# Performance work log

Measured on AMD Instinct MI355X. Metric: run time of the kernel, lower is better.

## Reference

```python
import jax, jax.numpy as jnp
import numpy as np

EMBED, HIDDEN, VOCAB = 512, 512, 30000
B, S, K, NT = 16, 128, 49, 5


def _lin(x, W, b):
    # torch nn.Linear: y = x @ W.T + b, W stored as (out, in)
    return x @ W.T + b


def setup_inputs() -> dict:
    key = jax.random.key(0)
    ks = jax.random.split(key, 32)
    g = lambda i, shape, scale=0.05: (jax.random.normal(ks[i], shape, dtype=jnp.float32) * scale)
    inp = {
        "epoch": 30,
        "h_t": jax.random.normal(ks[0], (B, S, HIDDEN), dtype=jnp.float32),
        "V": jax.random.normal(ks[1], (B, K, HIDDEN), dtype=jnp.float32),
        "T": jax.random.normal(ks[2], (B, NT, EMBED), dtype=jnp.float32),
        "W_ZV": g(3, (49, HIDDEN)), "b_ZV": jnp.zeros((49,), jnp.float32),
        "W_Zh": g(4, (49, HIDDEN)), "b_Zh": jnp.zeros((49,), jnp.float32),
        "W_az": g(5, (1, 49)), "b_az": jnp.zeros((1,), jnp.float32),
        "W_QT": g(6, (5, EMBED)), "b_QT": jnp.zeros((5,), jnp.float32),
        "W_Qh": g(7, (5, HIDDEN)), "b_Qh": jnp.zeros((5,), jnp.float32),
        "W_bq": g(8, (1, 5)), "b_bq": jnp.zeros((1,), jnp.float32),
        "W_sq": g(9, (EMBED, EMBED)), "b_sq": jnp.zeros((EMBED,), jnp.float32),
        "W_sh": g(10, (EMBED, HIDDEN)), "b_sh": jnp.zeros((EMBED,), jnp.float32),
        "W_Ss": g(11, (5, EMBED)), "b_Ss": jnp.zeros((5,), jnp.float32),
        "W_Sr": g(12, (5, EMBED)), "b_Sr": jnp.zeros((5,), jnp.float32),
        "W_sz": g(13, (EMBED, HIDDEN)), "b_sz": jnp.zeros((EMBED,), jnp.float32),
        "W_mlp": g(14, (VOCAB, EMBED)), "b_mlp": jnp.zeros((VOCAB,), jnp.float32),
    }
    return inp


def reference(epoch, h_t, V, T,
              W_ZV, b_ZV, W_Zh, b_Zh, W_az, b_az,
              W_QT, b_QT, W_Qh, b_Qh, W_bq, b_bq,
              W_sq, b_sq, W_sh, b_sh, W_Ss, b_Ss,
              W_Sr, b_Sr, W_sz, b_sz, W_mlp, b_mlp):
    # --- visual attention (dropout = identity, eval mode) ---
    # content_V: [B, S, K, 49]
    content_V = _lin(V, W_ZV, b_ZV)[:, None, :, :] + _lin(h_t, W_Zh, b_Zh)[:, :, None, :]
    visual_t = (jnp.tanh(content_V) @ W_az.T + b_az)[..., 0]          # [B, S, K]
    alpha_t = jax.nn.softmax(visual_t, axis=-1)
    z_t = jnp.einsum('bsk,bkh->bsh', alpha_t, V)                      # [B, S, H]
    r_t = jnp.tanh(_lin(z_t, W_sz, b_sz))                             # [B, S, E]
    # --- topic attention ---
    content_T = _lin(T, W_QT, b_QT)[:, None, :, :] + _lin(h_t, W_Qh, b_Qh)[:, :, None, :]  # [B,S,5,5]
    topic_t = (jnp.tanh(content_T) @ W_bq.T + b_bq)[..., 0]           # [B, S, 5]
    beta_t = jax.nn.softmax(topic_t, axis=-1)
    q_t = jnp.einsum('bst,bte->bse', beta_t, T)                       # [B, S, E]
    s_t = jnp.tanh(_lin(q_t, W_sq, b_sq) + _lin(h_t, W_sh, b_sh))     # [B, S, E]
    # --- sentinel scores: the torch loop reduces to (batch 0, diagonal pos) only ---
    qh0 = _lin(h_t[0], W_Qh, b_Qh)                                    # [S, 5]
    score_s = jnp.tanh(_lin(s_t[0], W_Ss, b_Ss) + qh0) @ W_bq.T + b_bq  # [S, 1]
    score_r = jnp.tanh(_lin(r_t[0], W_Sr, b_Sr) + qh0) @ W_bq.T + b_bq  # [S, 1]
    if epoch <= 20:
        gama_t = 1.0
    else:
        gama_t = jax.nn.sigmoid(score_s - score_r)[None, :, :]        # [1, S, 1]
    c_t = gama_t * s_t + (1.0 - gama_t) * r_t                         # [B, S, E]
    scores = _lin(c_t, W_mlp, b_mlp)                                  # [B, S, vocab]
    return scores
```

## Files before the change

### kernel.cpp

```cpp
#include <hip/hip_runtime.h>
#include <hip/hip_bf16.h>


typedef short bf16x8 __attribute__((ext_vector_type(8)));
typedef float f32x4 __attribute__((ext_vector_type(4)));
typedef short short8 __attribute__((ext_vector_type(8)));

static __device__ __forceinline__ short f2bf(float f) {
    union { float f; unsigned u; } v; v.f = f;
    unsigned r = v.u + 0x7FFFu + ((v.u >> 16) & 1u);
    return (short)(r >> 16);
}

#define GLD_LDS16(gp, lp)                                                          \
    __builtin_amdgcn_global_load_lds(                                              \
        (const __attribute__((address_space(1))) unsigned int*)(gp),               \
        (__attribute__((address_space(3))) unsigned int*)(lp), 16, 0, 0)

__global__ __launch_bounds__(256) void k_front(
    const float* __restrict__ h, const float* __restrict__ V, const float* __restrict__ T,
    const float* __restrict__ W_Zh, const float* __restrict__ W_Qh,
    const float* __restrict__ W_ZV, const float* __restrict__ W_QT,
    short* __restrict__ P1, short* __restrict__ P2, short* __restrict__ P3,
    short* __restrict__ V_b, short* __restrict__ T_b, short* __restrict__ h_b,
    const float* __restrict__ wsz, short* __restrict__ wsz_b,
    const float* __restrict__ wsq, short* __restrict__ wsq_b,
    const float* __restrict__ wsh, short* __restrict__ wsh_b,
    const float* __restrict__ wmlp, short* __restrict__ wmlp_b)
{
    const int bid = blockIdx.x;
    const int t = threadIdx.x;

    if (bid < 48) {
        const int pid = bid >> 4, blk = bid & 15;
        short* dst = (pid == 0) ? P1 : (pid == 1) ? P2 : P3;
        const int base = blk * 2048 + t * 8;
        const int r = base >> 9, c = base & 511;
        const float* srow = nullptr;
        if (pid == 0)      srow = (r < 49) ? (W_Zh + r * 512) : ((r < 54) ? (W_Qh + (r - 49) * 512) : nullptr);
        else if (pid == 1) srow = (r < 49) ? (W_ZV + r * 512) : nullptr;
        else               srow = (r < 5)  ? (W_QT + r * 512) : nullptr;
        short8 o = {0, 0, 0, 0, 0, 0, 0, 0};
        if (srow) {
            const float4 a = *(const float4*)(srow + c);
            const float4 b = *(const float4*)(srow + c + 4);
            o[0] = f2bf(a.x); o[1] = f2bf(a.y); o[2] = f2bf(a.z); o[3] = f2bf(a.w);
            o[4] = f2bf(b.x); o[5] = f2bf(b.y); o[6] = f2bf(b.z); o[7] = f2bf(b.w);
        }
        *(short8*)(dst + base) = o;
        return;
    }
    const float* src; short* dst; int i;
    if (bid < 244)       { src = V;    dst = V_b;    i = (bid - 48) * 256 + t; }
    else if (bid < 264)  { src = T;    dst = T_b;    i = (bid - 244) * 256 + t; }
    else if (bid < 776)  { src = h;    dst = h_b;    i = (bid - 264) * 256 + t; }
    else if (bid < 904)  { src = wsz;  dst = wsz_b;  i = (bid - 776) * 256 + t; }
    else if (bid < 1032) { src = wsq;  dst = wsq_b;  i = (bid - 904) * 256 + t; }
    else if (bid < 1160) { src = wsh;  dst = wsh_b;  i = (bid - 1032) * 256 + t; }
    else                 { src = wmlp; dst = wmlp_b; i = (bid - 1160) * 256 + t; }
    const float4 a = ((const float4*)src)[i * 2];
    const float4 b = ((const float4*)src)[i * 2 + 1];
    short8 o;
    o[0] = f2bf(a.x); o[1] = f2bf(a.y); o[2] = f2bf(a.z); o[3] = f2bf(a.w);
    o[4] = f2bf(b.x); o[5] = f2bf(b.y); o[6] = f2bf(b.z); o[7] = f2bf(b.w);
    ((short8*)dst)[i] = o;
}

__global__ __launch_bounds__(256) void k_linhv(
    const short* __restrict__ h_b, const short* __restrict__ V_b, const short* __restrict__ T_b,
    const short* __restrict__ P1, const short* __restrict__ P2, const short* __restrict__ P3,
    const float* __restrict__ b_Zh, const float* __restrict__ b_Qh,
    const float* __restrict__ b_ZV, const float* __restrict__ b_QT,
    float* __restrict__ Zh, float* __restrict__ Qh,
    float* __restrict__ ZV, float* __restrict__ QT)
{
    constexpr int K = 512;
    const int bid = blockIdx.x;
    int sect, m0;
    const short *Ag, *Wg;
    if (bid < 32)      { sect = 0; m0 = bid * 64;        Ag = h_b; Wg = P1; }
    else if (bid < 45) { sect = 1; m0 = (bid - 32) * 64; Ag = V_b; Wg = P2; }
    else               { sect = 2; m0 = (bid - 45) * 64; Ag = T_b; Wg = P3; }

    __shared__ __align__(16) short sA[64 * 64];
    __shared__ __align__(16) short sW[64 * 64];
    const int tid = threadIdx.x;
    const int l = tid & 63, w = tid >> 6;
    const int wm = (w & 1) * 32, wn = (w >> 1) * 32;
    const int lm = l & 15, lg = l >> 4;
    const int sr = l >> 3, sc = l & 7;
    f32x4 acc[2][2] = {};

    for (int k0 = 0; k0 < K; k0 += 64) {
        #pragma unroll
        for (int c = 0; c < 2; ++c) {
            const int R = w * 16 + c * 8;
            const int row = R + sr;
            GLD_LDS16(Ag + (size_t)(m0 + row) * K + k0 + ((sc ^ (row & 7)) << 3), sA + R * 64);
            GLD_LDS16(Wg + (size_t)row * K + k0 + ((sc ^ (row & 7)) << 3), sW + R * 64);
        }
        __syncthreads();
        bf16x8 af[2][2], bv[2][2];
        #pragma unroll
        for (int s = 0; s < 2; ++s)
            #pragma unroll
            for (int i = 0; i < 2; ++i) {
                const int ra = wm + i * 16 + lm;
                const int rb = wn + i * 16 + lm;
                af[s][i] = *(const bf16x8*)(sA + ra * 64 + (((s * 4 + lg) ^ (ra & 7)) << 3));
                bv[s][i] = *(const bf16x8*)(sW + rb * 64 + (((s * 4 + lg) ^ (rb & 7)) << 3));
            }
        #pragma unroll
        for (int s = 0; s < 2; ++s)
            #pragma unroll
            for (int i = 0; i < 2; ++i)
                #pragma unroll
                for (int j = 0; j < 2; ++j)
                    acc[i][j] = __builtin_amdgcn_mfma_f32_16x16x32_bf16(af[s][i], bv[s][j], acc[i][j], 0, 0, 0);
        __syncthreads();
    }

    #pragma unroll
    for (int j = 0; j < 2; ++j) {
        const int n = wn + j * 16 + lm;
        #pragma unroll
        for (int i = 0; i < 2; ++i) {
            #pragma unroll
            for (int q = 0; q < 4; ++q) {
                const int m = m0 + wm + i * 16 + lg * 4 + q;
                const float v = acc[i][j][q];
                if (sect == 0) {
                    if (n < 49)      Zh[(size_t)m * 64 + n] = v + b_Zh[n];
                    else if (n < 54) Qh[(size_t)m * 8 + (n - 49)] = v + b_Qh[n - 49];
                } else if (sect == 1) {
                    if (m < 784 && n < 49) ZV[(size_t)m * 64 + n] = v + b_ZV[n];
                } else {
                    if (m < 80 && n < 5) QT[(size_t)m * 8 + n] = v + b_QT[n];
                }
            }
        }
    }
}

__global__ void k_attn(const float* __restrict__ V, const float* __restrict__ T,
                       const float* __restrict__ ZV, const float* __restrict__ Zh,
                       const float* __restrict__ QT, const float* __restrict__ Qh,
                       const float* __restrict__ W_az, const float* __restrict__ b_az,
                       const float* __restrict__ W_bq, const float* __restrict__ b_bq,
                       short* __restrict__ z_bf, short* __restrict__ q_bf)
{
    const int row = blockIdx.x;
    const int b = row >> 7;
    const int t = threadIdx.x;
    __shared__ float zh[49], waz[49], alpha[49], beta[5];
    if (t < 49) { zh[t] = Zh[row * 64 + t]; waz[t] = W_az[t]; }
    __syncthreads();
    if (t < 49) {
        const float* zv = ZV + (b * 49 + t) * 64;
        float acc = b_az[0];
        for (int j = 0; j < 49; ++j) acc += tanhf(zv[j] + zh[j]) * waz[j];
        alpha[t] = acc;
    } else if (t >= 64 && t < 69) {
        const int tt = t - 64;
        const float* qt = QT + (b * 5 + tt) * 8;
        const float* qh = Qh + row * 8;
        float acc = b_bq[0];
        for (int j = 0; j < 5; ++j) acc += tanhf(qt[j] + qh[j]) * W_bq[j];
        beta[tt] = acc;
    }
    __syncthreads();
    const int wv = t >> 6, l = t & 63;
    if (wv == 0) {
        float a = (l < 49) ? alpha[l] : -1e30f;
        float m = a;
        #pragma unroll
        for (int off = 32; off; off >>= 1) m = fmaxf(m, __shfl_xor(m, off));
        float e = (l < 49) ? expf(a - m) : 0.f;
        float s = e;
        #pragma unroll
        for (int off = 32; off; off >>= 1) s += __shfl_xor(s, off);
        if (l < 49) alpha[l] = e / s;
    } else if (wv == 1) {
        float a = (l < 5) ? beta[l] : -1e30f;
        float m = a;
        #pragma unroll
        for (int off = 32; off; off >>= 1) m = fmaxf(m, __shfl_xor(m, off));
        float e = (l < 5) ? expf(a - m) : 0.f;
        float s = e;
        #pragma unroll
        for (int off = 32; off; off >>= 1) s += __shfl_xor(s, off);
        if (l < 5) beta[l] = e / s;
    }
    __syncthreads();
    const float* Vb = V + (size_t)b * 49 * 512;
    const float* Tb = T + (size_t)b * 5 * 512;
    for (int hd = t; hd < 512; hd += 256) {
        float az = 0.f;
        #pragma unroll
        for (int k = 0; k < 49; ++k) az = fmaf(alpha[k], Vb[k * 512 + hd], az);
        z_bf[(size_t)row * 512 + hd] = f2bf(az);
        float aq = 0.f;
        #pragma unroll
        for (int k = 0; k < 5; ++k) aq = fmaf(beta[k], Tb[k * 512 + hd], aq);
        q_bf[(size_t)row * 512 + hd] = f2bf(aq);
    }
}

__global__ __launch_bounds__(256) void k_rs(
    const short* __restrict__ Zb, const short* __restrict__ Qb, const short* __restrict__ Hb,
    const short* __restrict__ Wsz, const short* __restrict__ Wsq, const short* __restrict__ Wsh,
    const float* __restrict__ b_sz, const float* __restrict__ b_sq, const float* __restrict__ b_sh,
    float* __restrict__ r_t, float* __restrict__ s_t)
{
    constexpr int K = 512, NN = 512;
    __shared__ __align__(16) short sA[64 * 64];
    __shared__ __align__(16) short sW[64 * 64];
    const int tid = threadIdx.x;
    const int l = tid & 63, w = tid >> 6;
    const int m0 = blockIdx.x * 64, n0 = blockIdx.y * 64;
    const int wm = (w & 1) * 32, wn = (w >> 1) * 32;
    const int lm = l & 15, lg = l >> 4;
    const int sr = l >> 3, sc = l & 7;
    f32x4 accr[2][2] = {}, accs[2][2] = {};

#define RS_PASS(AG, WG, ACC)                                                      \
    for (int k0 = 0; k0 < K; k0 += 64) {                                          \
        _Pragma("unroll")                                                         \
        for (int c = 0; c < 2; ++c) {                                             \
            const int R = w * 16 + c * 8;                                         \
            const int row = R + sr;                                               \
            GLD_LDS16((AG) + (size_t)(m0 + row) * K + k0 + ((sc ^ (row & 7)) << 3), sA + R * 64); \
            GLD_LDS16((WG) + (size_t)(n0 + row) * K + k0 + ((sc ^ (row & 7)) << 3), sW + R * 64); \
        }                                                                         \
        __syncthreads();                                                          \
        bf16x8 af[2][2], bv[2][2];                                                \
        _Pragma("unroll")                                                         \
        for (int s = 0; s < 2; ++s)                                               \
            _Pragma("unroll")                                                     \
            for (int i = 0; i < 2; ++i) {                                         \
                const int ra = wm + i * 16 + lm;                                  \
                const int rb = wn + i * 16 + lm;                                  \
                af[s][i] = *(const bf16x8*)(sA + ra * 64 + (((s * 4 + lg) ^ (ra & 7)) << 3)); \
                bv[s][i] = *(const bf16x8*)(sW + rb * 64 + (((s * 4 + lg) ^ (rb & 7)) << 3)); \
            }                                                                     \
        _Pragma("unroll")                                                         \
        for (int s = 0; s < 2; ++s)                                               \
            _Pragma("unroll")                                                     \
            for (int i = 0; i < 2; ++i)                                           \
                _Pragma("unroll")                                                 \
                for (int j = 0; j < 2; ++j)                                       \
                    ACC[i][j] = __builtin_amdgcn_mfma_f32_16x16x32_bf16(af[s][i], bv[s][j], ACC[i][j], 0, 0, 0); \
        __syncthreads();                                                          \
    }

    RS_PASS(Zb, Wsz, accr)
    RS_PASS(Qb, Wsq, accs)
    RS_PASS(Hb, Wsh, accs)
#undef RS_PASS

    #pragma unroll
    for (int j = 0; j < 2; ++j) {
        const int n = n0 + wn + j * 16 + lm;
        const float br = b_sz[n];
        const float bs = b_sq[n] + b_sh[n];
        #pragma unroll
        for (int i = 0; i < 2; ++i) {
            const int m = m0 + wm + i * 16 + lg * 4;
            #pragma unroll
            for (int q = 0; q < 4; ++q) {
                r_t[(size_t)(m + q) * NN + n] = tanhf(accr[i][j][q] + br);
                s_t[(size_t)(m + q) * NN + n] = tanhf(accs[i][j][q] + bs);
            }
        }
    }
}

__global__ __launch_bounds__(256, 4) void k_gemm_mlp(
    const short* __restrict__ A, const short* __restrict__ Wb,
    const float* __restrict__ bias, float* __restrict__ C)
{
    constexpr int N = 30000, K = 512;
    __shared__ __align__(16) short shA[128 * 64];
    __shared__ __align__(16) short shW[128 * 64];
    const int tid = threadIdx.x;
    const int l = tid & 63, w = tid >> 6;
    const int bid = blockIdx.x;
    const int swz = (bid & 7) * 470 + (bid >> 3);
    const int m0 = (swz & 15) * 128;
    const int n0 = (swz >> 4) * 128;
    const int wm = (w & 1) * 64, wn = (w >> 1) * 64;
    const int lm = l & 15, lg = l >> 4;
    const int sr = tid >> 3, sc = tid & 7;
    const short* Ag = A  + (size_t)m0 * K;
    const short* Wg = Wb + (size_t)n0 * K;
    f32x4 acc[4][4] = {};

    for (int t = 0; t < 8; ++t) {
        const int kk = t * 64;
        #pragma unroll
        for (int c = 0; c < 4; ++c) {
            const int row = c * 32 + sr;
            GLD_LDS16(Ag + (size_t)row * K + kk + ((sc ^ (row & 7)) << 3),
                      &shA[(c * 32 + w * 8) * 64]);
            GLD_LDS16(Wg + (size_t)row * K + kk + ((sc ^ (row & 7)) << 3),
                      &shW[(c * 32 + w * 8) * 64]);
        }
        __syncthreads();
        bf16x8 af[2][4], bv[2][4];
        #pragma unroll
        for (int s = 0; s < 2; ++s)
            #pragma unroll
            for (int i = 0; i < 4; ++i) {
                const int ra = wm + i * 16 + lm;
                const int rb = wn + i * 16 + lm;
                const int ck = s * 4 + lg;
                af[s][i] = *(const bf16x8*)(&shA[ra * 64 + ((ck ^ (ra & 7)) << 3)]);
                bv[s][i] = *(const bf16x8*)(&shW[rb * 64 + ((ck ^ (rb & 7)) << 3)]);
            }
        #pragma unroll
        for (int s = 0; s < 2; ++s)
            #pragma unroll
            for (int i = 0; i < 4; ++i)
                #pragma unroll
                for (int j = 0; j < 4; ++j)
                    acc[i][j] = __builtin_amdgcn_mfma_f32_16x16x32_bf16(
                        af[s][i], bv[s][j], acc[i][j], 0, 0, 0);
        __syncthreads();
    }

    #pragma unroll
    for (int j = 0; j < 4; ++j) {
        const int n = n0 + wn + j * 16 + lm;
        if (n >= N) continue;
        const float bj = bias[n];
        #pragma unroll
        for (int i = 0; i < 4; ++i) {
            const int m = m0 + wm + i * 16 + lg * 4;
            #pragma unroll
            for (int q = 0; q < 4; ++q)
                __builtin_nontemporal_store(acc[i][j][q] + bj, &C[(size_t)(m + q) * N + n]);
        }
    }
}

__global__ __launch_bounds__(256) void k_blend_gate(
    const float* __restrict__ s_t, const float* __restrict__ r_t,
    const float* __restrict__ Qh,
    const float* __restrict__ W_Ss, const float* __restrict__ b_Ss,
    const float* __restrict__ W_Sr, const float* __restrict__ b_Sr,
    const float* __restrict__ W_bq, const float* __restrict__ b_bq,
    const int* __restrict__ epoch, short* __restrict__ c_bf)
{
    const int row = blockIdx.x;
    const int s = row & 127;
    const int t = threadIdx.x;
    float g = 1.0f;
    if (epoch[0] > 20) {
        const int l = t & 63;
        const int d = l * 8;
        const float4 s0 = *(const float4*)(s_t + (size_t)s * 512 + d);
        const float4 s1 = *(const float4*)(s_t + (size_t)s * 512 + d + 4);
        const float4 r0 = *(const float4*)(r_t + (size_t)s * 512 + d);
        const float4 r1 = *(const float4*)(r_t + (size_t)s * 512 + d + 4);
        float ss = b_bq[0], sr = b_bq[0];
        #pragma unroll
        for (int k = 0; k < 5; ++k) {
            const float4 w0 = *(const float4*)(W_Ss + k * 512 + d);
            const float4 w1 = *(const float4*)(W_Ss + k * 512 + d + 4);
            const float4 v0 = *(const float4*)(W_Sr + k * 512 + d);
            const float4 v1 = *(const float4*)(W_Sr + k * 512 + d + 4);
            float as = s0.x*w0.x + s0.y*w0.y + s0.z*w0.z + s0.w*w0.w
                     + s1.x*w1.x + s1.y*w1.y + s1.z*w1.z + s1.w*w1.w;
            float ar = r0.x*v0.x + r0.y*v0.y + r0.z*v0.z + r0.w*v0.w
                     + r1.x*v1.x + r1.y*v1.y + r1.z*v1.z + r1.w*v1.w;
            #pragma unroll
            for (int off = 32; off; off >>= 1) {
                as += __shfl_xor(as, off);
                ar += __shfl_xor(ar, off);
            }
            const float qh = Qh[s * 8 + k];
            ss += tanhf(as + b_Ss[k] + qh) * W_bq[k];
            sr += tanhf(ar + b_Sr[k] + qh) * W_bq[k];
        }
        g = 1.f / (1.f + expf(-(ss - sr)));
    }
    const size_t base = (size_t)row * 512;
    for (int i = t; i < 512; i += 256)
        c_bf[base + i] = f2bf(g * s_t[base + i] + (1.f - g) * r_t[base + i]);
}

extern "C" void kernel_launch(void* const* d_in, const int* in_sizes, int n_in,
                              void* d_out, int out_size, void* d_ws, size_t ws_size,
                              hipStream_t stream)
{
    const int*   epoch = (const int*)  d_in[0];
    const float* h_t   = (const float*)d_in[1];
    const float* V     = (const float*)d_in[2];
    const float* T     = (const float*)d_in[3];
    const float* W_ZV  = (const float*)d_in[4];  const float* b_ZV = (const float*)d_in[5];
    const float* W_Zh  = (const float*)d_in[6];  const float* b_Zh = (const float*)d_in[7];
    const float* W_az  = (const float*)d_in[8];  const float* b_az = (const float*)d_in[9];
    const float* W_QT  = (const float*)d_in[10]; const float* b_QT = (const float*)d_in[11];
    const float* W_Qh  = (const float*)d_in[12]; const float* b_Qh = (const float*)d_in[13];
    const float* W_bq  = (const float*)d_in[14]; const float* b_bq = (const float*)d_in[15];
    const float* W_sq  = (const float*)d_in[16]; const float* b_sq = (const float*)d_in[17];
    const float* W_sh  = (const float*)d_in[18]; const float* b_sh = (const float*)d_in[19];
    const float* W_Ss  = (const float*)d_in[20]; const float* b_Ss = (const float*)d_in[21];
    const float* W_Sr  = (const float*)d_in[22]; const float* b_Sr = (const float*)d_in[23];
    const float* W_sz  = (const float*)d_in[24]; const float* b_sz = (const float*)d_in[25];
    const float* W_mlp = (const float*)d_in[26]; const float* b_mlp= (const float*)d_in[27];

    float* out = (float*)d_out;
    float* ws  = (float*)d_ws;
    const size_t M1 = 1024 * 1024;
    float* r_t  = ws;
    float* s_t  = ws + M1;
    float* Zh   = ws + 2 * M1;
    float* ZV   = Zh + 2048 * 64;
    float* Qh   = ZV + 784 * 64;
    float* QT   = Qh + 2048 * 8;
    float* pad  = QT + 80 * 8;
    short* sreg = (short*)(pad + 128);
    short* z_bf   = sreg;
    short* q_bf   = z_bf + M1;
    short* h_bf   = q_bf + M1;
    short* c_bf   = h_bf + M1;
    short* Wsz_bf = c_bf + M1;
    short* Wsq_bf = Wsz_bf + 512 * 512;
    short* Wsh_bf = Wsq_bf + 512 * 512;
    short* V_bf   = Wsh_bf + 512 * 512;
    short* T_bf   = V_bf + 832 * 512;
    short* P1     = T_bf + 128 * 512;
    short* P2     = P1 + 64 * 512;
    short* P3     = P2 + 64 * 512;
    short* W_bf   = P3 + 64 * 512;

    k_front<<<8660, 256, 0, stream>>>(h_t, V, T, W_Zh, W_Qh, W_ZV, W_QT,
                                      P1, P2, P3, V_bf, T_bf, h_bf,
                                      W_sz, Wsz_bf, W_sq, Wsq_bf, W_sh, Wsh_bf,
                                      W_mlp, W_bf);
    k_linhv<<<47, 256, 0, stream>>>(h_bf, V_bf, T_bf, P1, P2, P3,
                                    b_Zh, b_Qh, b_ZV, b_QT, Zh, Qh, ZV, QT);
    k_attn<<<2048, 256, 0, stream>>>(V, T, ZV, Zh, QT, Qh, W_az, b_az, W_bq, b_bq, z_bf, q_bf);
    k_rs<<<dim3(32, 8), 256, 0, stream>>>(z_bf, q_bf, h_bf, Wsz_bf, Wsq_bf, Wsh_bf,
                                          b_sz, b_sq, b_sh, r_t, s_t);
    k_blend_gate<<<2048, 256, 0, stream>>>(s_t, r_t, Qh, W_Ss, b_Ss, W_Sr, b_Sr,
                                           W_bq, b_bq, epoch, c_bf);
    k_gemm_mlp<<<3760, 256, 0, stream>>>(c_bf, W_bf, b_mlp, out);
}
```

Before: 177.6 us.

## Fuse gated blend into r/s GEMM epilogue, computing gate from batch-0 rows first

The r/s projection GEMM is split into two launches. A small first launch (grid 2x8) computes r_t and s_t only for the batch-0 rows, which are all the gate needs. A tiny per-position kernel then computes the sigmoid gate. The full GEMM applies the blend in its epilogue and writes bf16 c directly. This removes the full fp32 r_t/s_t write and re-read and the separate blend kernel, at the cost of recomputing the batch-0 tile and adding two small serialized launches.

```diff
diff --git a/kernel.cpp b/kernel.cpp
--- a/kernel.cpp
+++ b/kernel.cpp
@@ -206,11 +206,13 @@
     }
 }
 
-__global__ __launch_bounds__(256) void k_rs(
+template<bool FUSE>
+__global__ __launch_bounds__(256) void k_rs2(
     const short* __restrict__ Zb, const short* __restrict__ Qb, const short* __restrict__ Hb,
     const short* __restrict__ Wsz, const short* __restrict__ Wsq, const short* __restrict__ Wsh,
     const float* __restrict__ b_sz, const float* __restrict__ b_sq, const float* __restrict__ b_sh,
-    float* __restrict__ r_t, float* __restrict__ s_t)
+    const float* __restrict__ gama, const int* __restrict__ epoch,
+    float* __restrict__ r_t, float* __restrict__ s_t, short* __restrict__ c_bf)
 {
     constexpr int K = 512, NN = 512;
     __shared__ __align__(16) short sA[64 * 64];
@@ -258,6 +260,7 @@
     RS_PASS(Hb, Wsh, accs)
 #undef RS_PASS
 
+    const int ep = FUSE ? epoch[0] : 0;
     #pragma unroll
     for (int j = 0; j < 2; ++j) {
         const int n = n0 + wn + j * 16 + lm;
@@ -268,11 +271,56 @@
             const int m = m0 + wm + i * 16 + lg * 4;
             #pragma unroll
             for (int q = 0; q < 4; ++q) {
-                r_t[(size_t)(m + q) * NN + n] = tanhf(accr[i][j][q] + br);
-                s_t[(size_t)(m + q) * NN + n] = tanhf(accs[i][j][q] + bs);
+                const float rv = tanhf(accr[i][j][q] + br);
+                const float sv = tanhf(accs[i][j][q] + bs);
+                if (FUSE) {
+                    const float g = (ep > 20) ? gama[(m + q) & 127] : 1.0f;
+                    c_bf[(size_t)(m + q) * NN + n] = f2bf(g * sv + (1.f - g) * rv);
+                } else {
+                    r_t[(size_t)(m + q) * NN + n] = rv;
+                    s_t[(size_t)(m + q) * NN + n] = sv;
+                }
             }
         }
     }
+}
+
+__global__ __launch_bounds__(64) void k_gate(
+    const float* __restrict__ s_t, const float* __restrict__ r_t,
+    const float* __restrict__ Qh,
+    const float* __restrict__ W_Ss, const float* __restrict__ b_Ss,
+    const float* __restrict__ W_Sr, const float* __restrict__ b_Sr,
+    const float* __restrict__ W_bq, const float* __restrict__ b_bq,
+    const int* __restrict__ epoch, float* __restrict__ gama)
+{
+    const int s = blockIdx.x, l = threadIdx.x;
+    if (epoch[0] <= 20) { if (l == 0) gama[s] = 1.0f; return; }
+    const int d = l * 8;
+    const float4 s0 = *(const float4*)(s_t + (size_t)s * 512 + d);
+    const float4 s1 = *(const float4*)(s_t + (size_t)s * 512 + d + 4);
+    const float4 r0 = *(const float4*)(r_t + (size_t)s * 512 + d);
+    const float4 r1 = *(const float4*)(r_t + (size_t)s * 512 + d + 4);
+    float ss = b_bq[0], sr = b_bq[0];
+    #pragma unroll
+    for (int k = 0; k < 5; ++k) {
+        const float4 w0 = *(const float4*)(W_Ss + k * 512 + d);
+        const float4 w1 = *(const float4*)(W_Ss + k * 512 + d + 4);
+        const float4 v0 = *(const float4*)(W_Sr + k * 512 + d);
+        const float4 v1 = *(const float4*)(W_Sr + k * 512 + d + 4);
+        float as = s0.x*w0.x + s0.y*w0.y + s0.z*w0.z + s0.w*w0.w
+                 + s1.x*w1.x + s1.y*w1.y + s1.z*w1.z + s1.w*w1.w;
+        float ar = r0.x*v0.x + r0.y*v0.y + r0.z*v0.z + r0.w*v0.w
+                 + r1.x*v1.x + r1.y*v1.y + r1.z*v1.z + r1.w*v1.w;
+        #pragma unroll
+        for (int off = 32; off; off >>= 1) {
+            as += __shfl_xor(as, off);
+            ar += __shfl_xor(ar, off);
+        }
+        const float qh = Qh[s * 8 + k];
+        ss += tanhf(as + b_Ss[k] + qh) * W_bq[k];
+        sr += tanhf(ar + b_Sr[k] + qh) * W_bq[k];
+    }
+    if (l == 0) gama[s] = 1.f / (1.f + expf(-(ss - sr)));
 }
 
 __global__ __launch_bounds__(256, 4) void k_gemm_mlp(
@@ -341,52 +389,6 @@
                 __builtin_nontemporal_store(acc[i][j][q] + bj, &C[(size_t)(m + q) * N + n]);
         }
     }
-}
-
-__global__ __launch_bounds__(256) void k_blend_gate(
-    const float* __restrict__ s_t, const float* __restrict__ r_t,
-    const float* __restrict__ Qh,
-    const float* __restrict__ W_Ss, const float* __restrict__ b_Ss,
-    const float* __restrict__ W_Sr, const float* __restrict__ b_Sr,
-    const float* __restrict__ W_bq, const float* __restrict__ b_bq,
-    const int* __restrict__ epoch, short* __restrict__ c_bf)
-{
-    const int row = blockIdx.x;
-    const int s = row & 127;
-    const int t = threadIdx.x;
-    float g = 1.0f;
-    if (epoch[0] > 20) {
-        const int l = t & 63;
-        const int d = l * 8;
-        const float4 s0 = *(const float4*)(s_t + (size_t)s * 512 + d);
-        const float4 s1 = *(const float4*)(s_t + (size_t)s * 512 + d + 4);
-        const float4 r0 = *(const float4*)(r_t + (size_t)s * 512 + d);
-        const float4 r1 = *(const float4*)(r_t + (size_t)s * 512 + d + 4);
-        float ss = b_bq[0], sr = b_bq[0];
-        #pragma unroll
-        for (int k = 0; k < 5; ++k) {
-            const float4 w0 = *(const float4*)(W_Ss + k * 512 + d);
-            const float4 w1 = *(const float4*)(W_Ss + k * 512 + d + 4);
-            const float4 v0 = *(const float4*)(W_Sr + k * 512 + d);
-            const float4 v1 = *(const float4*)(W_Sr + k * 512 + d + 4);
-            float as = s0.x*w0.x + s0.y*w0.y + s0.z*w0.z + s0.w*w0.w
-                     + s1.x*w1.x + s1.y*w1.y + s1.z*w1.z + s1.w*w1.w;
-            float ar = r0.x*v0.x + r0.y*v0.y + r0.z*v0.z + r0.w*v0.w
-                     + r1.x*v1.x + r1.y*v1.y + r1.z*v1.z + r1.w*v1.w;
-            #pragma unroll
-            for (int off = 32; off; off >>= 1) {
-                as += __shfl_xor(as, off);
-                ar += __shfl_xor(ar, off);
-            }
-            const float qh = Qh[s * 8 + k];
-            ss += tanhf(as + b_Ss[k] + qh) * W_bq[k];
-            sr += tanhf(ar + b_Sr[k] + qh) * W_bq[k];
-        }
-        g = 1.f / (1.f + expf(-(ss - sr)));
-    }
-    const size_t base = (size_t)row * 512;
-    for (int i = t; i < 512; i += 256)
-        c_bf[base + i] = f2bf(g * s_t[base + i] + (1.f - g) * r_t[base + i]);
 }
 
 extern "C" void kernel_launch(void* const* d_in, const int* in_sizes, int n_in,
@@ -419,8 +421,8 @@
     float* ZV   = Zh + 2048 * 64;
     float* Qh   = ZV + 784 * 64;
     float* QT   = Qh + 2048 * 8;
-    float* pad  = QT + 80 * 8;
-    short* sreg = (short*)(pad + 128);
+    float* gama = QT + 80 * 8;
+    short* sreg = (short*)(gama + 128);
     short* z_bf   = sreg;
     short* q_bf   = z_bf + M1;
     short* h_bf   = q_bf + M1;
@@ -442,9 +444,13 @@
     k_linhv<<<47, 256, 0, stream>>>(h_bf, V_bf, T_bf, P1, P2, P3,
                                     b_Zh, b_Qh, b_ZV, b_QT, Zh, Qh, ZV, QT);
     k_attn<<<2048, 256, 0, stream>>>(V, T, ZV, Zh, QT, Qh, W_az, b_az, W_bq, b_bq, z_bf, q_bf);
-    k_rs<<<dim3(32, 8), 256, 0, stream>>>(z_bf, q_bf, h_bf, Wsz_bf, Wsq_bf, Wsh_bf,
-                                          b_sz, b_sq, b_sh, r_t, s_t);
-    k_blend_gate<<<2048, 256, 0, stream>>>(s_t, r_t, Qh, W_Ss, b_Ss, W_Sr, b_Sr,
-                                           W_bq, b_bq, epoch, c_bf);
+    k_rs2<false><<<dim3(2, 8), 256, 0, stream>>>(z_bf, q_bf, h_bf, Wsz_bf, Wsq_bf, Wsh_bf,
+                                                 b_sz, b_sq, b_sh, nullptr, epoch,
+                                                 r_t, s_t, nullptr);
+    k_gate<<<128, 64, 0, stream>>>(s_t, r_t, Qh, W_Ss, b_Ss, W_Sr, b_Sr,
+                                   W_bq, b_bq, epoch, gama);
+    k_rs2<true><<<dim3(32, 8), 256, 0, stream>>>(z_bf, q_bf, h_bf, Wsz_bf, Wsq_bf, Wsh_bf,
+                                                 b_sz, b_sq, b_sh, gama, epoch,
+                                                 nullptr, nullptr, c_bf);
     k_gemm_mlp<<<3760, 256, 0, stream>>>(c_bf, W_bf, b_mlp, out);
 }
```

After: 190.1 us. 7.1% more time.

## Move weight bf16 conversions from front kernel into attention kernel launch

Applied to the files above, without the earlier changes.

Weight fp32-to-bf16 conversions (W_sz, W_sq, W_sh, W_mlp) move out of the front kernel and become extra blocks appended to the attention kernel grid. The small k_linhv kernel no longer waits behind the large W_mlp conversion. The conversion work now runs alongside the attention rows, so it can overlap with that latency-bound phase. The weights are still converted on every call, and the order still satisfies the later kernels' dependencies.

```diff
diff --git a/kernel.cpp b/kernel.cpp
--- a/kernel.cpp
+++ b/kernel.cpp
@@ -10,6 +10,16 @@
     union { float f; unsigned u; } v; v.f = f;
     unsigned r = v.u + 0x7FFFu + ((v.u >> 16) & 1u);
     return (short)(r >> 16);
+}
+
+static __device__ __forceinline__ void cvt_blk(const float* __restrict__ src,
+                                               short* __restrict__ dst, int i) {
+    const float4 a = ((const float4*)src)[i * 2];
+    const float4 b = ((const float4*)src)[i * 2 + 1];
+    short8 o;
+    o[0] = f2bf(a.x); o[1] = f2bf(a.y); o[2] = f2bf(a.z); o[3] = f2bf(a.w);
+    o[4] = f2bf(b.x); o[5] = f2bf(b.y); o[6] = f2bf(b.z); o[7] = f2bf(b.w);
+    ((short8*)dst)[i] = o;
 }
 
 #define GLD_LDS16(gp, lp)                                                          \
@@ -22,11 +32,7 @@
     const float* __restrict__ W_Zh, const float* __restrict__ W_Qh,
     const float* __restrict__ W_ZV, const float* __restrict__ W_QT,
     short* __restrict__ P1, short* __restrict__ P2, short* __restrict__ P3,
-    short* __restrict__ V_b, short* __restrict__ T_b, short* __restrict__ h_b,
-    const float* __restrict__ wsz, short* __restrict__ wsz_b,
-    const float* __restrict__ wsq, short* __restrict__ wsq_b,
-    const float* __restrict__ wsh, short* __restrict__ wsh_b,
-    const float* __restrict__ wmlp, short* __restrict__ wmlp_b)
+    short* __restrict__ V_b, short* __restrict__ T_b, short* __restrict__ h_b)
 {
     const int bid = blockIdx.x;
     const int t = threadIdx.x;
@@ -50,20 +56,9 @@
         *(short8*)(dst + base) = o;
         return;
     }
-    const float* src; short* dst; int i;
-    if (bid < 244)       { src = V;    dst = V_b;    i = (bid - 48) * 256 + t; }
-    else if (bid < 264)  { src = T;    dst = T_b;    i = (bid - 244) * 256 + t; }
-    else if (bid < 776)  { src = h;    dst = h_b;    i = (bid - 264) * 256 + t; }
-    else if (bid < 904)  { src = wsz;  dst = wsz_b;  i = (bid - 776) * 256 + t; }
-    else if (bid < 1032) { src = wsq;  dst = wsq_b;  i = (bid - 904) * 256 + t; }
-    else if (bid < 1160) { src = wsh;  dst = wsh_b;  i = (bid - 1032) * 256 + t; }
-    else                 { src = wmlp; dst = wmlp_b; i = (bid - 1160) * 256 + t; }
-    const float4 a = ((const float4*)src)[i * 2];
-    const float4 b = ((const float4*)src)[i * 2 + 1];
-    short8 o;
-    o[0] = f2bf(a.x); o[1] = f2bf(a.y); o[2] = f2bf(a.z); o[3] = f2bf(a.w);
-    o[4] = f2bf(b.x); o[5] = f2bf(b.y); o[6] = f2bf(b.z); o[7] = f2bf(b.w);
-    ((short8*)dst)[i] = o;
+    if (bid < 244)      cvt_blk(V, V_b, (bid - 48) * 256 + t);
+    else if (bid < 264) cvt_blk(T, T_b, (bid - 244) * 256 + t);
+    else                cvt_blk(h, h_b, (bid - 264) * 256 + t);
 }
 
 __global__ __launch_bounds__(256) void k_linhv(
@@ -147,11 +142,23 @@
                        const float* __restrict__ QT, const float* __restrict__ Qh,
                        const float* __restrict__ W_az, const float* __restrict__ b_az,
                        const float* __restrict__ W_bq, const float* __restrict__ b_bq,
-                       short* __restrict__ z_bf, short* __restrict__ q_bf)
-{
-    const int row = blockIdx.x;
+                       short* __restrict__ z_bf, short* __restrict__ q_bf,
+                       const float* __restrict__ wsz, short* __restrict__ wsz_b,
+                       const float* __restrict__ wsq, short* __restrict__ wsq_b,
+                       const float* __restrict__ wsh, short* __restrict__ wsh_b,
+                       const float* __restrict__ wmlp, short* __restrict__ wmlp_b)
+{
+    const int bid = blockIdx.x;
+    const int t = threadIdx.x;
+    if (bid >= 2048) {
+        if (bid < 2176)      cvt_blk(wsz, wsz_b, (bid - 2048) * 256 + t);
+        else if (bid < 2304) cvt_blk(wsq, wsq_b, (bid - 2176) * 256 + t);
+        else if (bid < 2432) cvt_blk(wsh, wsh_b, (bid - 2304) * 256 + t);
+        else                 cvt_blk(wmlp, wmlp_b, (bid - 2432) * 256 + t);
+        return;
+    }
+    const int row = bid;
     const int b = row >> 7;
-    const int t = threadIdx.x;
     __shared__ float zh[49], waz[49], alpha[49], beta[5];
     if (t < 49) { zh[t] = Zh[row * 64 + t]; waz[t] = W_az[t]; }
     __syncthreads();
@@ -435,13 +442,14 @@
     short* P3     = P2 + 64 * 512;
     short* W_bf   = P3 + 64 * 512;
 
-    k_front<<<8660, 256, 0, stream>>>(h_t, V, T, W_Zh, W_Qh, W_ZV, W_QT,
-                                      P1, P2, P3, V_bf, T_bf, h_bf,
-                                      W_sz, Wsz_bf, W_sq, Wsq_bf, W_sh, Wsh_bf,
-                                      W_mlp, W_bf);
+    k_front<<<776, 256, 0, stream>>>(h_t, V, T, W_Zh, W_Qh, W_ZV, W_QT,
+                                     P1, P2, P3, V_bf, T_bf, h_bf);
     k_linhv<<<47, 256, 0, stream>>>(h_bf, V_bf, T_bf, P1, P2, P3,
                                     b_Zh, b_Qh, b_ZV, b_QT, Zh, Qh, ZV, QT);
-    k_attn<<<2048, 256, 0, stream>>>(V, T, ZV, Zh, QT, Qh, W_az, b_az, W_bq, b_bq, z_bf, q_bf);
+    k_attn<<<9932, 256, 0, stream>>>(V, T, ZV, Zh, QT, Qh, W_az, b_az, W_bq, b_bq,
+                                     z_bf, q_bf,
+                                     W_sz, Wsz_bf, W_sq, Wsq_bf, W_sh, Wsh_bf,
+                                     W_mlp, W_bf);
     k_rs<<<dim3(32, 8), 256, 0, stream>>>(z_bf, q_bf, h_bf, Wsz_bf, Wsq_bf, Wsh_bf,
                                           b_sz, b_sq, b_sh, r_t, s_t);
     k_blend_gate<<<2048, 256, 0, stream>>>(s_t, r_t, Qh, W_Ss, b_Ss, W_Sr, b_Sr,
```

After: 177.7 us. Within noise of the previous version (+0.1%).
